# Kernel tuning notes

Hardware: AMD Instinct MI355X
Metric: run time of the kernel (lower is better)

The kernel has to match this reference:

```python
import jax, jax.numpy as jnp
import numpy as np

EMB_DIM = 16

def _pos_enc_table(side_len, emb_dim):
    pos = np.arange(side_len)[:, None].astype(np.float64)
    j = np.arange(emb_dim)[None, :]
    enc = pos / np.power(10000.0, 2.0 * (j // 2) / emb_dim)
    enc[0, :] = 0.0
    enc[1:, 0::2] = np.sin(enc[1:, 0::2])
    enc[1:, 1::2] = np.cos(enc[1:, 1::2])
    return enc.astype(np.float32)  # [L, E]

def _pos_embeddings(side_len, emb_dim):
    t = _pos_enc_table(side_len, emb_dim)
    # original uses raw .view (row-major reshape), NOT a transpose
    x = np.tile(t.reshape(1, emb_dim, side_len, 1), (1, 1, 1, side_len))
    y = np.tile(t.reshape(1, emb_dim, 1, side_len), (1, 1, side_len, 1))
    return jnp.asarray(np.concatenate((x, y), axis=1))  # [1, 2E, L, L]

def setup_inputs() -> dict:
    key = jax.random.key(0)
    ks = jax.random.split(key, 7)
    B, C, L = 32, 224, 32
    Cin = C + 2 * EMB_DIM  # 256
    K = V = 256
    s = 0.02
    return {
        "x": jax.random.normal(ks[0], (B, C, L, L), dtype=jnp.float32),
        "wq": jax.random.normal(ks[1], (K, Cin), dtype=jnp.float32) * s,
        "bq": jax.random.normal(ks[2], (K,), dtype=jnp.float32) * s,
        "wk": jax.random.normal(ks[3], (K, Cin), dtype=jnp.float32) * s,
        "bk": jax.random.normal(ks[4], (K,), dtype=jnp.float32) * s,
        "wv": jax.random.normal(ks[5], (V, Cin), dtype=jnp.float32) * s,
        "bv": jax.random.normal(ks[6], (V,), dtype=jnp.float32) * s,
    }

def reference(x, wq, bq, wk, bk, wv, bv):
    B, C, H, W = x.shape
    S = H * W
    Kdim = wq.shape[0]
    Vdim = wv.shape[0]
    pe = _pos_embeddings(H, EMB_DIM).astype(x.dtype)  # [1, 2E, H, W]
    x0 = jnp.concatenate([x, jnp.broadcast_to(pe, (B, 2 * EMB_DIM, H, W))], axis=1)
    x0 = x0.reshape(B, C + 2 * EMB_DIM, S)  # [B, Cin, S]
    # 1x1 conv == channel matmul, then ReLU nonlin
    q = jax.nn.relu(jnp.einsum('kc,bcs->bks', wq, x0) + bq[None, :, None])
    k = jax.nn.relu(jnp.einsum('kc,bcs->bks', wk, x0) + bk[None, :, None])
    v = jax.nn.relu(jnp.einsum('vc,bcs->bvs', wv, x0) + bv[None, :, None])
    attn = jnp.einsum('bks,bkt->bst', q, k) / jnp.sqrt(jnp.asarray(Kdim, x.dtype))
    mask = jnp.tril(jnp.ones((S, S), dtype=x.dtype))  # causal incl. self
    attn = attn * mask + (1.0 - mask) * (-10000.0)
    attn = jax.nn.softmax(attn, axis=-1) * mask  # double masking as in source
    out1 = jnp.einsum('bst,bvt->bvs', attn, v)  # [B, V, S]
    # NOTE: source computes out1 + fc(out1) but then overwrites with out1.view(...)
    return out1.reshape(B, Vdim, H, W)
```

## Files before the change

### kernel.cpp

```cpp
#include <hip/hip_runtime.h>
#include <cstdint>

typedef float  f32x4  __attribute__((ext_vector_type(4)));
typedef short  short8 __attribute__((ext_vector_type(8)));
typedef _Float16 half4 __attribute__((ext_vector_type(4)));
typedef _Float16 half8 __attribute__((ext_vector_type(8)));

__device__ __forceinline__ unsigned short f2bf(float f) {
    unsigned u = __builtin_bit_cast(unsigned, f);
    u += 0x7FFFu + ((u >> 16) & 1u);
    return (unsigned short)(u >> 16);
}

__global__ void wconv_kernel(const float* __restrict__ wq,
                             const float* __restrict__ wk,
                             const float* __restrict__ wv,
                             unsigned short* __restrict__ Wb) {
    int p = blockIdx.x >> 8;
    int i = ((blockIdx.x & 255) << 8) + threadIdx.x;
    const float* src = (p == 0) ? wq : ((p == 1) ? wk : wv);
    Wb[(p << 16) + i] = f2bf(src[i]);
}

__global__ __launch_bounds__(256, 2) void fproj_kernel(
        const float* __restrict__ x,
        const unsigned short* __restrict__ Wb,
        const float* __restrict__ bq, const float* __restrict__ bk,
        const float* __restrict__ bv,
        unsigned short* __restrict__ Q, unsigned short* __restrict__ K,
        _Float16* __restrict__ V) {
    __shared__ __align__(16) char Xlds[32768];
    __shared__ __align__(16) char Wlds[32768];
    float* Tt = (float*)Wlds;

    int st = blockIdx.x;
    int b  = blockIdx.y;
    int sb = st << 6;
    int tid = threadIdx.x; int w = tid >> 6; int l = tid & 63;
    int g = l >> 4, c = l & 15;
    int wr = w >> 1, wc = w & 1;

    #pragma unroll 1
    for (int sc = 0; sc < 2; ++sc) {
        if (sc) __syncthreads();
        #pragma unroll
        for (int r = 0; r < 28; ++r) {
            int idx = r * 256 + tid;
            int cc = idx >> 5, lo = idx & 31;
            Tt[cc * 33 + lo] = x[((b * 224 + cc) << 10) + sb + (sc << 5) + lo];
        }
        __syncthreads();
        #pragma unroll
        for (int r = 0; r < 4; ++r) {
            int idx = r * 256 + tid;
            if (idx < 896) {
                int cc16 = idx >> 5;
                int sl = idx & 31;
                int s = (sc << 5) + sl;
                short8 v8;
                #pragma unroll
                for (int j = 0; j < 8; ++j)
                    v8[j] = (short)f2bf(Tt[(cc16 * 8 + j) * 33 + sl]);
                *(short8*)&Xlds[(s << 9) + ((cc16 ^ (s & 7)) << 4)] = v8;
            }
        }
        if (tid < 128) {
            int sl = tid >> 2;
            int cc16 = 28 + (tid & 3);
            int s = (sc << 5) + sl;
            int sg = sb + s;
            int h = sg >> 5, ww = sg & 31;
            short8 v8;
            #pragma unroll
            for (int j = 0; j < 8; ++j) {
                int ch = (cc16 - 28) * 8 + j;
                int i = (ch < 16) ? (ch * 32 + h) : ((ch - 16) * 32 + ww);
                int ll = i >> 4, e = i & 15;
                float val = 0.f;
                if (ll > 0) {
                    float ang = (float)ll * powf(10000.f, -(float)(e >> 1) * 0.125f);
                    val = (e & 1) ? cosf(ang) : sinf(ang);
                }
                v8[j] = (short)f2bf(val);
            }
            *(short8*)&Xlds[(s << 9) + ((cc16 ^ (s & 7)) << 4)] = v8;
        }
    }
    __syncthreads();

    short8 af[2][8];
    #pragma unroll
    for (int i = 0; i < 2; ++i) {
        const char* ab = &Xlds[(wr * 32 + i * 16 + c) << 9];
        #pragma unroll
        for (int kk = 0; kk < 8; ++kk)
            af[i][kk] = *(const short8*)&ab[((kk * 4 + g) ^ (c & 7)) << 4];
    }

    #pragma unroll 1
    for (int pj = 0; pj < 3; ++pj) {
        const float* bias = (pj == 0) ? bq : ((pj == 1) ? bk : bv);
        #pragma unroll 1
        for (int ot = 0; ot < 4; ++ot) {
            const unsigned short* Wg = Wb + (pj << 16) + (ot << 14);
            #pragma unroll
            for (int p = 0; p < 8; ++p) {
                int ch = p * 256 + tid;
                int row = ch >> 5;
                int cl = (ch & 31) ^ (row & 7);
                __builtin_amdgcn_global_load_lds(
                    (const unsigned int*)&Wg[(row << 8) + cl * 8],
                    (unsigned int*)(Wlds + ((p << 8) + (w << 6)) * 16), 16, 0, 0);
            }
            asm volatile("s_waitcnt vmcnt(0)\n\ts_barrier" ::: "memory");

            f32x4 acc[2][2];
            #pragma unroll
            for (int i = 0; i < 2; ++i)
                #pragma unroll
                for (int j = 0; j < 2; ++j) acc[i][j] = (f32x4){0.f, 0.f, 0.f, 0.f};

            const char* bb0 = &Wlds[(wc * 32 + c) << 9];
            const char* bb1 = &Wlds[(wc * 32 + 16 + c) << 9];
            __builtin_amdgcn_s_setprio(1);
            #pragma unroll
            for (int kk = 0; kk < 8; ++kk) {
                int co = ((kk * 4 + g) ^ (c & 7)) << 4;
                short8 b0 = *(const short8*)&bb0[co];
                short8 b1 = *(const short8*)&bb1[co];
                acc[0][0] = __builtin_amdgcn_mfma_f32_16x16x32_bf16(af[0][kk], b0, acc[0][0], 0, 0, 0);
                acc[0][1] = __builtin_amdgcn_mfma_f32_16x16x32_bf16(af[0][kk], b1, acc[0][1], 0, 0, 0);
                acc[1][0] = __builtin_amdgcn_mfma_f32_16x16x32_bf16(af[1][kk], b0, acc[1][0], 0, 0, 0);
                acc[1][1] = __builtin_amdgcn_mfma_f32_16x16x32_bf16(af[1][kk], b1, acc[1][1], 0, 0, 0);
            }
            __builtin_amdgcn_s_setprio(0);

            #pragma unroll
            for (int j = 0; j < 2; ++j) {
                int o = (ot << 6) + wc * 32 + j * 16 + c;
                float bbv = bias[o];
                #pragma unroll
                for (int i = 0; i < 2; ++i) {
                    int sgb = sb + wr * 32 + i * 16;
                    if (pj < 2) {
                        unsigned short* dst = (pj == 0) ? Q : K;
                        #pragma unroll
                        for (int r = 0; r < 4; ++r) {
                            float v = fmaxf(acc[i][j][r] + bbv, 0.f);
                            int s = sgb + 4 * g + r;
                            dst[(((b << 10) + s) << 8) + o] = f2bf(v);
                        }
                    } else {
                        half4 hv;
                        #pragma unroll
                        for (int r = 0; r < 4; ++r)
                            hv[r] = (_Float16)fmaxf(acc[i][j][r] + bbv, 0.f);
                        int hi = (sgb >> 4) & 1;
                        *(half4*)&V[(((b << 8) + o) << 10) + ((sgb >> 5) << 5)
                                    + (g << 3) + (hi << 2)] = hv;
                    }
                }
            }
            __syncthreads();
        }
    }
}

__global__ __launch_bounds__(256, 2) void attn_kernel(
        const unsigned short* __restrict__ Q,
        const unsigned short* __restrict__ K,
        const _Float16* __restrict__ V,
        float* __restrict__ out) {
    __shared__ __align__(16) char Klds[2][16384];
    __shared__ __align__(16) char Vlds[2][16384];

    int bid = blockIdx.x;
    int xcd  = bid & 7;
    int qv   = (bid >> 3) & 7;
    int bhi  = (bid >> 6) & 3;
    int hf   = bid >> 8;
    int b  = (bhi << 3) | xcd;
    int qt = hf ? qv : (15 - qv);

    int tid = threadIdx.x; int w = tid >> 6; int l = tid & 63;
    int g = l >> 4, c = l & 15;
    int s0 = (qt << 6) + (w << 4);

    short8 qf[8];
    #pragma unroll
    for (int kk = 0; kk < 8; ++kk)
        qf[kk] = *(const short8*)&Q[(((b << 10) + s0 + c) << 8) + kk * 32 + g * 8];

    float m = -1e30f, lsum = 0.f;
    f32x4 acc[16];
    #pragma unroll
    for (int i = 0; i < 16; ++i) acc[i] = (f32x4){0.f, 0.f, 0.f, 0.f};

    const unsigned short* Kb_ = &K[(size_t)b << 18];
    const _Float16*       Vb_ = &V[(size_t)b << 18];

    int nt = 2 * qt + 2;
    int dt = 2 * qt + (w >> 1);

    auto stage = [&](int t, int bufi) {
        int t0 = t << 5;
        #pragma unroll
        for (int j = 0; j < 4; ++j) {
            int ch = (j << 8) + tid;
            int trow = ch >> 5;
            int cl = (ch & 31) ^ (trow & 7);
            __builtin_amdgcn_global_load_lds(
                (const unsigned int*)&Kb_[((t0 + trow) << 8) + cl * 8],
                (unsigned int*)(Klds[bufi] + ((j << 8) + (w << 6)) * 16), 16, 0, 0);
        }
        #pragma unroll
        for (int j = 0; j < 4; ++j) {
            int ch = (j << 8) + tid;
            int v = ch >> 2;
            int gq = (ch & 3) ^ ((v >> 1) & 3);
            __builtin_amdgcn_global_load_lds(
                (const unsigned int*)&Vb_[(v << 10) + (t << 5) + gq * 8],
                (unsigned int*)(Vlds[bufi] + ((j << 8) + (w << 6)) * 16), 16, 0, 0);
        }
    };

    stage(0, 0);

    for (int t = 0; t < nt; ++t) {
        asm volatile("s_waitcnt vmcnt(0)\n\ts_barrier" ::: "memory");
        if (t + 1 < nt) stage(t + 1, (t + 1) & 1);
        if (t > dt) continue;

        const char* Kl = Klds[t & 1];
        const char* Vl = Vlds[t & 1];
        half8 vread[16];
        #pragma unroll
        for (int vt = 0; vt < 16; ++vt) {
            int pos = (vt << 6) + (c << 2) + (g ^ ((c >> 1) & 3));
            vread[vt] = *(const half8*)&Vl[pos << 4];
        }
        #pragma unroll
        for (int sub = 0; sub < 2; ++sub) {
            bool dmask = (t == dt) && (sub == (w & 1));
            if ((t == dt) && !(w & 1) && sub == 1) break;
            int toff = sub << 4;
            f32x4 sc0 = {0.f,0.f,0.f,0.f}, sc1 = {0.f,0.f,0.f,0.f};
            const char* kbase = &Kl[(toff + c) * 512];
            __builtin_amdgcn_s_setprio(1);
            #pragma unroll
            for (int kk = 0; kk < 8; kk += 2) {
                short8 a0 = *(const short8*)&kbase[(((kk * 4 + g)       ^ (c & 7)) << 4)];
                short8 a1 = *(const short8*)&kbase[((((kk + 1) * 4 + g) ^ (c & 7)) << 4)];
                sc0 = __builtin_amdgcn_mfma_f32_16x16x32_bf16(a0, qf[kk], sc0, 0, 0, 0);
                sc1 = __builtin_amdgcn_mfma_f32_16x16x32_bf16(a1, qf[kk + 1], sc1, 0, 0, 0);
            }
            __builtin_amdgcn_s_setprio(0);
            float sv[4];
            #pragma unroll
            for (int r = 0; r < 4; ++r) sv[r] = (sc0[r] + sc1[r]) * 0.0625f;
            if (dmask) {
                #pragma unroll
                for (int r = 0; r < 4; ++r)
                    if (4 * g + r > c) sv[r] = -1e30f;
            }
            float tm = fmaxf(fmaxf(sv[0], sv[1]), fmaxf(sv[2], sv[3]));
            if (!__all((int)(tm <= m + 8.f))) {
                float tr = fmaxf(tm, __shfl_xor(tm, 16));
                tr = fmaxf(tr, __shfl_xor(tr, 32));
                float mnew = fmaxf(m, tr);
                float alpha = __expf(m - mnew);
                m = mnew;
                lsum *= alpha;
                #pragma unroll
                for (int i = 0; i < 16; ++i) acc[i] *= alpha;
            }
            float p[4];
            #pragma unroll
            for (int r = 0; r < 4; ++r) { p[r] = __expf(sv[r] - m); lsum += p[r]; }
            half4 pb;
            #pragma unroll
            for (int r = 0; r < 4; ++r) pb[r] = (_Float16)p[r];
            __builtin_amdgcn_s_setprio(1);
            #pragma unroll
            for (int vt = 0; vt < 16; ++vt) {
                half4 vf;
                #pragma unroll
                for (int jj = 0; jj < 4; ++jj) vf[jj] = vread[vt][sub * 4 + jj];
                acc[vt] = __builtin_amdgcn_mfma_f32_16x16x16f16(vf, pb, acc[vt], 0, 0, 0);
            }
            __builtin_amdgcn_s_setprio(0);
        }
    }

    lsum += __shfl_xor(lsum, 16);
    lsum += __shfl_xor(lsum, 32);
    float rl = 1.f / lsum;
    #pragma unroll
    for (int vt = 0; vt < 16; ++vt) {
        #pragma unroll
        for (int r = 0; r < 4; ++r)
            out[(((b << 8) + vt * 16 + 4 * g + r) << 10) + s0 + c] = acc[vt][r] * rl;
    }
}

extern "C" void kernel_launch(void* const* d_in, const int* in_sizes, int n_in,
                              void* d_out, int out_size, void* d_ws, size_t ws_size,
                              hipStream_t stream) {
    const float* x  = (const float*)d_in[0];
    const float* wq = (const float*)d_in[1];
    const float* bq = (const float*)d_in[2];
    const float* wk = (const float*)d_in[3];
    const float* bk = (const float*)d_in[4];
    const float* wv = (const float*)d_in[5];
    const float* bv = (const float*)d_in[6];
    float* out = (float*)d_out;

    char* ws = (char*)d_ws;
    unsigned short* Wb = (unsigned short*)ws;
    unsigned short* Qb = (unsigned short*)(ws + 393216);
    unsigned short* Kb = (unsigned short*)(ws + 393216 + 16777216);
    _Float16*       Vb = (_Float16*)     (ws + 393216 + 2 * 16777216);

    wconv_kernel<<<768, 256, 0, stream>>>(wq, wk, wv, Wb);
    fproj_kernel<<<dim3(16, 32), 256, 0, stream>>>(x, Wb, bq, bk, bv, Qb, Kb, Vb);
    attn_kernel<<<512, 256, 0, stream>>>(Qb, Kb, Vb, out);
}
```

Measured before the change: 103.4 us.

## Double-buffer projection weight tiles and pre-swizzle V layout into tile blocks

The projection kernel now streams 32-row weight tiles into two alternating LDS buffers across a flattened 24-step loop. The next tile's load is issued before the current tile's MFMAs, overlapping weight fetch with compute and removing the trailing per-tile barrier. V is now stored in a tiled, pre-swizzled layout, one contiguous 8K-element block per 32 keys, so the attention kernel's V staging becomes a linear contiguous copy. The costs are smaller MFMA tiles per iteration, more iterations and barriers, and a redundant scalar store before the half4 V store.

```diff
diff --git a/kernel.cpp b/kernel.cpp
--- a/kernel.cpp
+++ b/kernel.cpp
@@ -30,7 +30,7 @@
         unsigned short* __restrict__ Q, unsigned short* __restrict__ K,
         _Float16* __restrict__ V) {
     __shared__ __align__(16) char Xlds[32768];
-    __shared__ __align__(16) char Wlds[32768];
+    __shared__ __align__(16) char Wlds[2][16384];
     float* Tt = (float*)Wlds;
 
     int st = blockIdx.x;
@@ -97,71 +97,68 @@
             af[i][kk] = *(const short8*)&ab[((kk * 4 + g) ^ (c & 7)) << 4];
     }
 
+    auto stageW = [&](int i, int bufi) {
+        const unsigned short* Wg = Wb + ((i >> 3) << 16) + ((i & 7) << 13);
+        #pragma unroll
+        for (int p = 0; p < 4; ++p) {
+            int ch = (p << 8) + tid;
+            int row = ch >> 5;
+            int cl = (ch & 31) ^ (row & 7);
+            __builtin_amdgcn_global_load_lds(
+                (const unsigned int*)&Wg[(row << 8) + cl * 8],
+                (unsigned int*)(Wlds[bufi] + ((p << 8) + (w << 6)) * 16), 16, 0, 0);
+        }
+    };
+
+    stageW(0, 0);
+
     #pragma unroll 1
-    for (int pj = 0; pj < 3; ++pj) {
+    for (int i = 0; i < 24; ++i) {
+        asm volatile("s_waitcnt vmcnt(0)\n\ts_barrier" ::: "memory");
+        if (i + 1 < 24) stageW(i + 1, (i + 1) & 1);
+        int pj = i >> 3;
         const float* bias = (pj == 0) ? bq : ((pj == 1) ? bk : bv);
-        #pragma unroll 1
-        for (int ot = 0; ot < 4; ++ot) {
-            const unsigned short* Wg = Wb + (pj << 16) + (ot << 14);
-            #pragma unroll
-            for (int p = 0; p < 8; ++p) {
-                int ch = p * 256 + tid;
-                int row = ch >> 5;
-                int cl = (ch & 31) ^ (row & 7);
-                __builtin_amdgcn_global_load_lds(
-                    (const unsigned int*)&Wg[(row << 8) + cl * 8],
-                    (unsigned int*)(Wlds + ((p << 8) + (w << 6)) * 16), 16, 0, 0);
-            }
-            asm volatile("s_waitcnt vmcnt(0)\n\ts_barrier" ::: "memory");
-
-            f32x4 acc[2][2];
-            #pragma unroll
-            for (int i = 0; i < 2; ++i)
-                #pragma unroll
-                for (int j = 0; j < 2; ++j) acc[i][j] = (f32x4){0.f, 0.f, 0.f, 0.f};
-
-            const char* bb0 = &Wlds[(wc * 32 + c) << 9];
-            const char* bb1 = &Wlds[(wc * 32 + 16 + c) << 9];
-            __builtin_amdgcn_s_setprio(1);
-            #pragma unroll
-            for (int kk = 0; kk < 8; ++kk) {
-                int co = ((kk * 4 + g) ^ (c & 7)) << 4;
-                short8 b0 = *(const short8*)&bb0[co];
-                short8 b1 = *(const short8*)&bb1[co];
-                acc[0][0] = __builtin_amdgcn_mfma_f32_16x16x32_bf16(af[0][kk], b0, acc[0][0], 0, 0, 0);
-                acc[0][1] = __builtin_amdgcn_mfma_f32_16x16x32_bf16(af[0][kk], b1, acc[0][1], 0, 0, 0);
-                acc[1][0] = __builtin_amdgcn_mfma_f32_16x16x32_bf16(af[1][kk], b0, acc[1][0], 0, 0, 0);
-                acc[1][1] = __builtin_amdgcn_mfma_f32_16x16x32_bf16(af[1][kk], b1, acc[1][1], 0, 0, 0);
-            }
-            __builtin_amdgcn_s_setprio(0);
-
-            #pragma unroll
-            for (int j = 0; j < 2; ++j) {
-                int o = (ot << 6) + wc * 32 + j * 16 + c;
-                float bbv = bias[o];
-                #pragma unroll
-                for (int i = 0; i < 2; ++i) {
-                    int sgb = sb + wr * 32 + i * 16;
-                    if (pj < 2) {
-                        unsigned short* dst = (pj == 0) ? Q : K;
-                        #pragma unroll
-                        for (int r = 0; r < 4; ++r) {
-                            float v = fmaxf(acc[i][j][r] + bbv, 0.f);
-                            int s = sgb + 4 * g + r;
-                            dst[(((b << 10) + s) << 8) + o] = f2bf(v);
-                        }
-                    } else {
-                        half4 hv;
-                        #pragma unroll
-                        for (int r = 0; r < 4; ++r)
-                            hv[r] = (_Float16)fmaxf(acc[i][j][r] + bbv, 0.f);
-                        int hi = (sgb >> 4) & 1;
-                        *(half4*)&V[(((b << 8) + o) << 10) + ((sgb >> 5) << 5)
-                                    + (g << 3) + (hi << 2)] = hv;
-                    }
+        const char* Wl = Wlds[i & 1];
+
+        f32x4 acc[2];
+        acc[0] = (f32x4){0.f, 0.f, 0.f, 0.f};
+        acc[1] = (f32x4){0.f, 0.f, 0.f, 0.f};
+        const char* bb = &Wl[(wc * 16 + c) << 9];
+        __builtin_amdgcn_s_setprio(1);
+        #pragma unroll
+        for (int kk = 0; kk < 8; ++kk) {
+            int co = ((kk * 4 + g) ^ (c & 7)) << 4;
+            short8 b0 = *(const short8*)&bb[co];
+            acc[0] = __builtin_amdgcn_mfma_f32_16x16x32_bf16(af[0][kk], b0, acc[0], 0, 0, 0);
+            acc[1] = __builtin_amdgcn_mfma_f32_16x16x32_bf16(af[1][kk], b0, acc[1], 0, 0, 0);
+        }
+        __builtin_amdgcn_s_setprio(0);
+
+        int o = ((i & 7) << 5) + (wc << 4) + c;
+        float bbv = bias[o];
+        #pragma unroll
+        for (int i2 = 0; i2 < 2; ++i2) {
+            int sgb = sb + wr * 32 + i2 * 16;
+            if (pj < 2) {
+                unsigned short* dst = (pj == 0) ? Q : K;
+                #pragma unroll
+                for (int r = 0; r < 4; ++r) {
+                    float v = fmaxf(acc[i2][r] + bbv, 0.f);
+                    int s = sgb + 4 * g + r;
+                    dst[(((b << 10) + s) << 8) + o] = f2bf(v);
                 }
-            }
-            __syncthreads();
+            } else {
+                half4 hv;
+                #pragma unroll
+                for (int r = 0; r < 4; ++r)
+                    hv[r] = (_Float16)fmaxf(acc[i2][r] + bbv, 0.f);
+                int hi = (sgb >> 4) & 1;
+                int tt = sgb >> 5;
+                V[((size_t)((b << 5) + tt) << 13)
+                  + ((o << 2) + (g ^ ((o >> 1) & 3))) * 8 + (hi << 2) + 0] = hv[0];
+                *(half4*)&V[((size_t)((b << 5) + tt) << 13)
+                  + ((o << 2) + (g ^ ((o >> 1) & 3))) * 8 + (hi << 2)] = hv;
+            }
         }
     }
 }
@@ -216,10 +213,8 @@
         #pragma unroll
         for (int j = 0; j < 4; ++j) {
             int ch = (j << 8) + tid;
-            int v = ch >> 2;
-            int gq = (ch & 3) ^ ((v >> 1) & 3);
             __builtin_amdgcn_global_load_lds(
-                (const unsigned int*)&Vb_[(v << 10) + (t << 5) + gq * 8],
+                (const unsigned int*)&Vb_[((size_t)t << 13) + ch * 8],
                 (unsigned int*)(Vlds[bufi] + ((j << 8) + (w << 6)) * 16), 16, 0, 0);
         }
     };
```

Measured after the change: 105.7 us. 2.2% more time.
